# Optimization experiments

Measured on AMD Instinct MI355X. Metric: run time of the kernel, lower is better.

Reference implementation:

```python
import jax, jax.numpy as jnp
from jax import lax
import numpy as np


def setup_inputs() -> dict:
    key = jax.random.key(0)
    k1, k2 = jax.random.split(key)
    sat_features = jax.random.normal(k1, (128, 4, 64, 16), dtype=jnp.float32)  # [B_s, h, w, c]
    grd_features = jax.random.normal(k2, (128, 4, 64, 16), dtype=jnp.float32)  # [B_g, h, gw, c]
    return {"sat_features": sat_features, "grd_features": grd_features}


def reference(sat_features, grd_features):
    B_s, h, w, c = sat_features.shape
    B_g, gh, gw, gc = grd_features.shape
    assert h == gh and c == gc

    # --- corr: circular cross-correlation over width via conv2d ---
    n = gw - 1
    sat_pad = jnp.concatenate([sat_features, sat_features[:, :, :n, :]], axis=2)  # [B_s,h,w+n,c]
    rhs = jnp.transpose(grd_features, (1, 2, 3, 0))  # HWIO: [h,gw,c,B_g]
    out = lax.conv_general_dilated(
        sat_pad, rhs, window_strides=(1, 1), padding='VALID',
        dimension_numbers=('NHWC', 'HWIO', 'NHWC'))  # [B_s,1,w,B_g]
    corr = out[:, 0, :, :]                  # [B_s, w, B_g]
    orien = jnp.argmax(corr, axis=1)        # [B_s, B_g] int

    # --- crop_sat: circular-shift gather along width, crop to grd width ---
    shift = orien % w                                                   # [B_s,B_g]
    idx = (jnp.arange(gw)[None, None, :] + shift[:, :, None]) % w       # [B_s,B_g,gw]
    # gather: sat_crop[i,j,y,k,ch] = sat_features[i, y, idx[i,j,k], ch]
    sat_crop = jnp.take_along_axis(
        sat_features[:, None],              # [B_s,1,h,w,c]
        idx[:, :, None, :, None],           # [B_s,B_g,1,gw,1]
        axis=3)                             # -> [B_s,B_g,h,gw,c]

    # --- L2 normalize per (sat,grd) pair and squared-chord distance ---
    norm = jnp.sqrt(jnp.sum(sat_crop * sat_crop, axis=(2, 3, 4), keepdims=True))
    sat_matrix = sat_crop / jnp.maximum(norm, 1e-12)
    dot = jnp.sum(sat_matrix * grd_features[None], axis=(2, 3, 4))      # [B_s,B_g]
    distance = 2.0 - 2.0 * dot.T                                        # [B_g,B_s]

    return sat_features, grd_features, distance, orien
```

## Files before the change

### kernel.cpp

```cpp
#include <hip/hip_runtime.h>
#include <math.h>

typedef _Float16 f16;
typedef __attribute__((ext_vector_type(8))) _Float16 f16x8;
typedef __attribute__((ext_vector_type(16))) float f32x16;

#define DIST_OFF  1048576
#define ORI_OFF   1064960
#define SATP_STR  72
#define RTS       68

#define MFMA(a,b,c) __builtin_amdgcn_mfma_f32_32x32x16_f16((a),(b),(c),0,0,0)
#define RIDX(g, j0) ((g) * RTS + ((j0) ^ ((((g) >> 3) & 1) << 4)))

__global__ __launch_bounds__(256) void prep_k(const float* __restrict__ grd,
                                              f16* __restrict__ gHi, f16* __restrict__ gLo) {
    __shared__ f16 tH[8192], tL[8192];
    const int b = blockIdx.x;
    const int tid = threadIdx.x;
    const int g0 = (b & 7) * 16;
    const int kq = b >> 3;
    #pragma unroll
    for (int i = 0; i < 32; ++i) {
        int flat = i * 256 + tid;
        int g_l = flat >> 9;
        int r   = flat & 511;
        int h   = r >> 7;
        int j   = r & 127;
        float v = grd[(((g0 + g_l) * 4 + h) * 64 + kq * 8) * 16 + j];
        int k_l = (j >> 4) * 64 + h * 16 + (j & 15);
        f16 hv = (f16)v;
        int a = (k_l >> 3) * 128 + g_l * 8 + (k_l & 7);
        tH[a] = hv;
        tL[a] = (f16)(v - (float)hv);
    }
    __syncthreads();
    #pragma unroll
    for (int i = 0; i < 4; ++i) {
        int f = i * 256 + tid;
        int dst = (kq * 64 + (f >> 4)) * 128 + g0 + (f & 15);
        ((f16x8*)gHi)[dst] = *(const f16x8*)(tH + f * 8);
        ((f16x8*)gLo)[dst] = *(const f16x8*)(tL + f * 8);
    }
}

__global__ __launch_bounds__(1024, 4) void corr_k(const float* __restrict__ sat,
                                                  const f16* __restrict__ gHi,
                                                  const f16* __restrict__ gLo,
                                                  float* __restrict__ out) {
    __shared__ __align__(16) unsigned char smem[69632];
    __shared__ float wred[16];
    __shared__ float rnormS;
    f16* sH = (f16*)smem;
    f16* sL = sH + 127 * SATP_STR;
    float* red = (float*)smem;

    const int tid = threadIdx.x;
    const int s  = blockIdx.x >> 1;
    const int gh = blockIdx.x & 1;
    const int wave = tid >> 6, lane = tid & 63;
    const int m = lane & 31, half = lane >> 5;

    const float* satS = sat + s * 4096;
    float ssq = 0.f;
    #pragma unroll
    for (int r = 0; r < 4; ++r) {
        int idx = r * 1024 + tid;
        float v = satS[idx];
        int h = idx >> 10, w = (idx >> 4) & 63, c = idx & 15;
        int col = h * 16 + c;
        f16 hv = (f16)v, lv = (f16)(v - (float)hv);
        sH[w * SATP_STR + col] = hv;
        sL[w * SATP_STR + col] = lv;
        if (w < 63) { sH[(w + 64) * SATP_STR + col] = hv; sL[(w + 64) * SATP_STR + col] = lv; }
        ssq += v * v;
    }
    #pragma unroll
    for (int off = 32; off > 0; off >>= 1) ssq += __shfl_down(ssq, off, 64);
    if (lane == 0) wred[wave] = ssq;
    __syncthreads();
    if (tid == 0) {
        float t = 0.f;
        #pragma unroll
        for (int i = 0; i < 16; ++i) t += wred[i];
        rnormS = 1.f / fmaxf(sqrtf(t), 1e-12f);
    }

    const f16* A0h = sH + m * SATP_STR + half * 8;
    const f16* A0l = sL + m * SATP_STR + half * 8;
    const f16x8* BHp = (const f16x8*)gHi;
    const f16x8* BLp = (const f16x8*)gLo;
    const int ggBase = half * 128 + gh * 64 + m;

    f32x16 acc[2][2];
    #pragma unroll
    for (int jt = 0; jt < 2; ++jt)
        #pragma unroll
        for (int gt = 0; gt < 2; ++gt)
            #pragma unroll
            for (int r = 0; r < 16; ++r) acc[jt][gt][r] = 0.f;

    const int t0 = wave * 16;
    #pragma unroll 4
    for (int t = t0; t < t0 + 16; ++t) {
        int ao = (t >> 2) * SATP_STR + (t & 3) * 16;
        f16x8 ah0 = *(const f16x8*)(A0h + ao);
        f16x8 ah1 = *(const f16x8*)(A0h + ao + 32 * SATP_STR);
        f16x8 al0 = *(const f16x8*)(A0l + ao);
        f16x8 al1 = *(const f16x8*)(A0l + ao + 32 * SATP_STR);
        int bu = t * 256 + ggBase;
        f16x8 bh0 = BHp[bu], bh1 = BHp[bu + 32];
        f16x8 bl0 = BLp[bu], bl1 = BLp[bu + 32];
        acc[0][0] = MFMA(ah0, bh0, acc[0][0]);
        acc[0][1] = MFMA(ah0, bh1, acc[0][1]);
        acc[1][0] = MFMA(ah1, bh0, acc[1][0]);
        acc[1][1] = MFMA(ah1, bh1, acc[1][1]);
        acc[0][0] = MFMA(ah0, bl0, acc[0][0]);
        acc[0][1] = MFMA(ah0, bl1, acc[0][1]);
        acc[1][0] = MFMA(ah1, bl0, acc[1][0]);
        acc[1][1] = MFMA(ah1, bl1, acc[1][1]);
        acc[0][0] = MFMA(al0, bh0, acc[0][0]);
        acc[0][1] = MFMA(al0, bh1, acc[0][1]);
        acc[1][0] = MFMA(al1, bh0, acc[1][0]);
        acc[1][1] = MFMA(al1, bh1, acc[1][1]);
    }

#define WTILE(T) { float* tp = red + (T) * 4352; \
    _Pragma("unroll") for (int jt = 0; jt < 2; ++jt) \
    _Pragma("unroll") for (int gt = 0; gt < 2; ++gt) { \
        int g = gt * 32 + m; \
        _Pragma("unroll") for (int q = 0; q < 4; ++q) { \
            int j0 = jt * 32 + 8 * q + 4 * half; \
            float4 v = { acc[jt][gt][4*q], acc[jt][gt][4*q+1], acc[jt][gt][4*q+2], acc[jt][gt][4*q+3] }; \
            *(float4*)(tp + RIDX(g, j0)) = v; } } }

#define ATILE(T) { const float* tp = red + (T) * 4352; \
    _Pragma("unroll") for (int jt = 0; jt < 2; ++jt) \
    _Pragma("unroll") for (int gt = 0; gt < 2; ++gt) { \
        int g = gt * 32 + m; \
        _Pragma("unroll") for (int q = 0; q < 4; ++q) { \
            int j0 = jt * 32 + 8 * q + 4 * half; \
            float4 v = *(const float4*)(tp + RIDX(g, j0)); \
            acc[jt][gt][4*q] += v.x; acc[jt][gt][4*q+1] += v.y; \
            acc[jt][gt][4*q+2] += v.z; acc[jt][gt][4*q+3] += v.w; } } }

    __syncthreads();
    if (wave >= 8 && wave < 12) WTILE(wave - 8)
    __syncthreads();
    if (wave < 4) ATILE(wave)
    __syncthreads();
    if (wave >= 12) WTILE(wave - 12)
    __syncthreads();
    if (wave >= 4 && wave < 8) ATILE(wave - 4)
    __syncthreads();
    if (wave >= 4 && wave < 8) WTILE(wave - 4)
    __syncthreads();
    if (wave < 4) ATILE(wave)
    __syncthreads();
    if (wave == 2 || wave == 3) WTILE(wave - 2)
    __syncthreads();
    if (wave < 2) ATILE(wave)
    __syncthreads();
    if (wave == 1) WTILE(0)
    __syncthreads();

    if (wave == 0) {
        ATILE(0)
        #pragma unroll
        for (int gt = 0; gt < 2; ++gt) {
            float best = -1e30f;
            int bj = 0;
            #pragma unroll
            for (int jt = 0; jt < 2; ++jt)
                #pragma unroll
                for (int q = 0; q < 4; ++q)
                    #pragma unroll
                    for (int i = 0; i < 4; ++i) {
                        int j = jt * 32 + 8 * q + 4 * half + i;
                        float v = acc[jt][gt][4 * q + i];
                        if (v > best) { best = v; bj = j; }
                    }
            float ob = __shfl_xor(best, 32, 64);
            int  obj = __shfl_xor(bj, 32, 64);
            if (ob > best || (ob == best && obj < bj)) { best = ob; bj = obj; }
            if ((half == 0) == (gt == 0)) {
                int g = gh * 64 + gt * 32 + m;
                float dot = best * rnormS;
                out[DIST_OFF + g * 128 + s] = 2.f - 2.f * dot;
                out[ORI_OFF + s * 128 + g]  = (float)bj;
            }
        }
    }
}

__global__ void copy_k(const float4* __restrict__ a, const float4* __restrict__ b,
                       float4* __restrict__ out) {
    int i = blockIdx.x * 256 + threadIdx.x;
    out[i] = a[i];
    out[131072 + i] = b[i];
}

extern "C" void kernel_launch(void* const* d_in, const int* in_sizes, int n_in,
                              void* d_out, int out_size, void* d_ws, size_t ws_size,
                              hipStream_t stream) {
    const float* sat = (const float*)d_in[0];
    const float* grd = (const float*)d_in[1];
    float* out = (float*)d_out;

    f16* gHi = (f16*)out;
    f16* gLo = (f16*)(out + 262144);

    prep_k<<<64, 256, 0, stream>>>(grd, gHi, gLo);
    corr_k<<<256, 1024, 0, stream>>>(sat, gHi, gLo, out);
    copy_k<<<512, 256, 0, stream>>>((const float4*)sat, (const float4*)grd, (float4*)out);
}
```

Baseline: 91.38 us.

## Fuse passthrough copy into corr kernel and flatten cross-wave reduction

When the workspace is large enough, the split-precision ground features are staged there instead of in the output buffer, which lets the sat/grd passthrough copy run inside the correlation kernel and removes the separate copy launch. The multi-round tree reduction across 16 waves, with many barriers, becomes two rounds into 8 shared buffers, a parallel sum over all threads, and a per-row argmax done by 64 threads. Each wave's K loop is rotated to spread out load patterns. In exchange, shared memory per block roughly doubles, which may cut occupancy, and the final argmax is a serial 64-element scan per thread.

After: 88.11 us. 3.6% less time.

```diff
diff --git a/kernel.cpp b/kernel.cpp
--- a/kernel.cpp
+++ b/kernel.cpp
@@ -8,10 +8,9 @@
 #define DIST_OFF  1048576
 #define ORI_OFF   1064960
 #define SATP_STR  72
-#define RTS       68
+#define RSTR      66
 
 #define MFMA(a,b,c) __builtin_amdgcn_mfma_f32_32x32x16_f16((a),(b),(c),0,0,0)
-#define RIDX(g, j0) ((g) * RTS + ((j0) ^ ((((g) >> 3) & 1) << 4)))
 
 __global__ __launch_bounds__(256) void prep_k(const float* __restrict__ grd,
                                               f16* __restrict__ gHi, f16* __restrict__ gLo) {
@@ -47,8 +46,11 @@
 __global__ __launch_bounds__(1024, 4) void corr_k(const float* __restrict__ sat,
                                                   const f16* __restrict__ gHi,
                                                   const f16* __restrict__ gLo,
-                                                  float* __restrict__ out) {
-    __shared__ __align__(16) unsigned char smem[69632];
+                                                  float* __restrict__ out,
+                                                  const float4* __restrict__ satIn,
+                                                  const float4* __restrict__ grdIn,
+                                                  int fuse) {
+    __shared__ __align__(16) unsigned char smem[135168];
     __shared__ float wred[16];
     __shared__ float rnormS;
     f16* sH = (f16*)smem;
@@ -60,6 +62,13 @@
     const int gh = blockIdx.x & 1;
     const int wave = tid >> 6, lane = tid & 63;
     const int m = lane & 31, half = lane >> 5;
+
+    if (fuse && tid < 512) {
+        float4* o4 = (float4*)out;
+        int i = blockIdx.x * 512 + tid;
+        o4[i] = satIn[i];
+        o4[131072 + i] = grdIn[i];
+    }
 
     const float* satS = sat + s * 4096;
     float ssq = 0.f;
@@ -86,11 +95,10 @@
         rnormS = 1.f / fmaxf(sqrtf(t), 1e-12f);
     }
 
-    const f16* A0h = sH + m * SATP_STR + half * 8;
-    const f16* A0l = sL + m * SATP_STR + half * 8;
-    const f16x8* BHp = (const f16x8*)gHi;
-    const f16x8* BLp = (const f16x8*)gLo;
-    const int ggBase = half * 128 + gh * 64 + m;
+    const f16* Ah = sH + m * SATP_STR + half * 8;
+    const f16* Al = sL + m * SATP_STR + half * 8;
+    const f16x8* BH = (const f16x8*)gHi + half * 128 + gh * 64 + m;
+    const f16x8* BL = (const f16x8*)gLo + half * 128 + gh * 64 + m;
 
     f32x16 acc[2][2];
     #pragma unroll
@@ -101,16 +109,18 @@
             for (int r = 0; r < 16; ++r) acc[jt][gt][r] = 0.f;
 
     const int t0 = wave * 16;
+    const int rot = (wave & 3) * 4;
     #pragma unroll 4
-    for (int t = t0; t < t0 + 16; ++t) {
+    for (int i = 0; i < 16; ++i) {
+        int t = t0 + ((i + rot) & 15);
         int ao = (t >> 2) * SATP_STR + (t & 3) * 16;
-        f16x8 ah0 = *(const f16x8*)(A0h + ao);
-        f16x8 ah1 = *(const f16x8*)(A0h + ao + 32 * SATP_STR);
-        f16x8 al0 = *(const f16x8*)(A0l + ao);
-        f16x8 al1 = *(const f16x8*)(A0l + ao + 32 * SATP_STR);
-        int bu = t * 256 + ggBase;
-        f16x8 bh0 = BHp[bu], bh1 = BHp[bu + 32];
-        f16x8 bl0 = BLp[bu], bl1 = BLp[bu + 32];
+        f16x8 ah0 = *(const f16x8*)(Ah + ao);
+        f16x8 ah1 = *(const f16x8*)(Ah + ao + 32 * SATP_STR);
+        f16x8 al0 = *(const f16x8*)(Al + ao);
+        f16x8 al1 = *(const f16x8*)(Al + ao + 32 * SATP_STR);
+        int bu = t * 256;
+        f16x8 bh0 = BH[bu], bh1 = BH[bu + 32];
+        f16x8 bl0 = BL[bu], bl1 = BL[bu + 32];
         acc[0][0] = MFMA(ah0, bh0, acc[0][0]);
         acc[0][1] = MFMA(ah0, bh1, acc[0][1]);
         acc[1][0] = MFMA(ah1, bh0, acc[1][0]);
@@ -125,71 +135,52 @@
         acc[1][1] = MFMA(al1, bh1, acc[1][1]);
     }
 
-#define WTILE(T) { float* tp = red + (T) * 4352; \
+    __syncthreads();
+#define PUT(rp, op) { \
     _Pragma("unroll") for (int jt = 0; jt < 2; ++jt) \
     _Pragma("unroll") for (int gt = 0; gt < 2; ++gt) { \
-        int g = gt * 32 + m; \
+        float* row = (rp) + (gt * 32 + m) * RSTR + jt * 32 + half * 4; \
         _Pragma("unroll") for (int q = 0; q < 4; ++q) { \
-            int j0 = jt * 32 + 8 * q + 4 * half; \
-            float4 v = { acc[jt][gt][4*q], acc[jt][gt][4*q+1], acc[jt][gt][4*q+2], acc[jt][gt][4*q+3] }; \
-            *(float4*)(tp + RIDX(g, j0)) = v; } } }
-
-#define ATILE(T) { const float* tp = red + (T) * 4352; \
-    _Pragma("unroll") for (int jt = 0; jt < 2; ++jt) \
-    _Pragma("unroll") for (int gt = 0; gt < 2; ++gt) { \
-        int g = gt * 32 + m; \
-        _Pragma("unroll") for (int q = 0; q < 4; ++q) { \
-            int j0 = jt * 32 + 8 * q + 4 * half; \
-            float4 v = *(const float4*)(tp + RIDX(g, j0)); \
-            acc[jt][gt][4*q] += v.x; acc[jt][gt][4*q+1] += v.y; \
-            acc[jt][gt][4*q+2] += v.z; acc[jt][gt][4*q+3] += v.w; } } }
-
-    __syncthreads();
-    if (wave >= 8 && wave < 12) WTILE(wave - 8)
-    __syncthreads();
-    if (wave < 4) ATILE(wave)
-    __syncthreads();
-    if (wave >= 12) WTILE(wave - 12)
-    __syncthreads();
-    if (wave >= 4 && wave < 8) ATILE(wave - 4)
-    __syncthreads();
-    if (wave >= 4 && wave < 8) WTILE(wave - 4)
-    __syncthreads();
-    if (wave < 4) ATILE(wave)
-    __syncthreads();
-    if (wave == 2 || wave == 3) WTILE(wave - 2)
-    __syncthreads();
-    if (wave < 2) ATILE(wave)
-    __syncthreads();
-    if (wave == 1) WTILE(0)
-    __syncthreads();
-
-    if (wave == 0) {
-        ATILE(0)
+            float2 u = { acc[jt][gt][4*q], acc[jt][gt][4*q+1] }; \
+            float2 v = { acc[jt][gt][4*q+2], acc[jt][gt][4*q+3] }; \
+            op(row + q * 8, u, v); } } }
+#define OPW(p, u, v)  { *(float2*)(p) = u; *(float2*)((p) + 2) = v; }
+#define OPA(p, u, v)  { float2 a = *(float2*)(p), b = *(float2*)((p) + 2); \
+                        a.x += u.x; a.y += u.y; b.x += v.x; b.y += v.y; \
+                        *(float2*)(p) = a; *(float2*)((p) + 2) = b; }
+
+    if (wave >= 8) PUT(red + (wave - 8) * 4224, OPW)
+    __syncthreads();
+    if (wave < 8)  PUT(red + wave * 4224, OPA)
+    __syncthreads();
+    {
+        int g = tid >> 4, q4 = (tid & 15) * 4;
+        int base = g * RSTR + q4;
+        float2 u = {0.f, 0.f}, v = {0.f, 0.f};
         #pragma unroll
-        for (int gt = 0; gt < 2; ++gt) {
-            float best = -1e30f;
-            int bj = 0;
-            #pragma unroll
-            for (int jt = 0; jt < 2; ++jt)
-                #pragma unroll
-                for (int q = 0; q < 4; ++q)
-                    #pragma unroll
-                    for (int i = 0; i < 4; ++i) {
-                        int j = jt * 32 + 8 * q + 4 * half + i;
-                        float v = acc[jt][gt][4 * q + i];
-                        if (v > best) { best = v; bj = j; }
-                    }
-            float ob = __shfl_xor(best, 32, 64);
-            int  obj = __shfl_xor(bj, 32, 64);
-            if (ob > best || (ob == best && obj < bj)) { best = ob; bj = obj; }
-            if ((half == 0) == (gt == 0)) {
-                int g = gh * 64 + gt * 32 + m;
-                float dot = best * rnormS;
-                out[DIST_OFF + g * 128 + s] = 2.f - 2.f * dot;
-                out[ORI_OFF + s * 128 + g]  = (float)bj;
-            }
+        for (int kh = 0; kh < 8; ++kh) {
+            float2 a = *(const float2*)(red + kh * 4224 + base);
+            float2 b = *(const float2*)(red + kh * 4224 + base + 2);
+            u.x += a.x; u.y += a.y; v.x += b.x; v.y += b.y;
         }
+        *(float2*)(red + base) = u;
+        *(float2*)(red + base + 2) = v;
+    }
+    __syncthreads();
+
+    if (tid < 64) {
+        int g = tid;
+        const float* row = red + g * RSTR;
+        float best = row[0];
+        int bj = 0;
+        for (int j = 1; j < 64; ++j) {
+            float v = row[j];
+            if (v > best) { best = v; bj = j; }
+        }
+        float dot = best * rnormS;
+        int gg = gh * 64 + g;
+        out[DIST_OFF + gg * 128 + s] = 2.f - 2.f * dot;
+        out[ORI_OFF + s * 128 + gg]  = (float)bj;
     }
 }
 
@@ -207,10 +198,21 @@
     const float* grd = (const float*)d_in[1];
     float* out = (float*)d_out;
 
-    f16* gHi = (f16*)out;
-    f16* gLo = (f16*)(out + 262144);
+    const bool useWs = (ws_size >= (size_t)2 * 1024 * 1024);
+    f16* gHi;
+    f16* gLo;
+    if (useWs) {
+        gHi = (f16*)d_ws;
+        gLo = gHi + 524288;
+    } else {
+        gHi = (f16*)out;
+        gLo = (f16*)(out + 262144);
+    }
 
     prep_k<<<64, 256, 0, stream>>>(grd, gHi, gLo);
-    corr_k<<<256, 1024, 0, stream>>>(sat, gHi, gLo, out);
-    copy_k<<<512, 256, 0, stream>>>((const float4*)sat, (const float4*)grd, (float4*)out);
-}
+    corr_k<<<256, 1024, 0, stream>>>(sat, gHi, gLo, out,
+                                     (const float4*)sat, (const float4*)grd,
+                                     useWs ? 1 : 0);
+    if (!useWs)
+        copy_k<<<512, 256, 0, stream>>>((const float4*)sat, (const float4*)grd, (float4*)out);
+}
```
